# Kernel optimization log

Hardware: AMD Instinct MI355X
Metric: run time of the kernel (lower is better)

The kernel has to match this reference:

```python
import jax, jax.numpy as jnp
import numpy as np
import math

D_MODEL = 1024
D_INNER = 2048
D_HALF = D_INNER // 2
D_STATE = 16
D_CONV = 4
DT_RANK = 64
B_SZ = 4
L = 2048


def _dw_conv(x, w, b):
    # x: (b, l, c), w: (k, 1, c) depthwise, SAME padding
    y = jax.lax.conv_general_dilated(
        x, w, window_strides=(1,), padding='SAME',
        feature_group_count=x.shape[-1],
        dimension_numbers=('NWC', 'WIO', 'NWC'))
    return y + b


def _selective_scan(u, delta, A, Bc, Cc, D):
    # u, delta: (b, l, d); Bc, Cc: (b, l, n); A: (d, n); D: (d,)
    b, l, d = u.shape
    n = A.shape[1]

    def step(h, inp):
        d_t, u_t, B_t, C_t = inp  # (b,d), (b,d), (b,n), (b,n)
        dA = jnp.exp(d_t[..., None] * A)                     # (b,d,n)
        h = dA * h + (d_t * u_t)[..., None] * B_t[:, None, :]
        y = jnp.einsum('bdn,bn->bd', h, C_t)
        return h, y

    h0 = jnp.zeros((b, d, n), u.dtype)
    xs = (jnp.moveaxis(delta, 1, 0), jnp.moveaxis(u, 1, 0),
          jnp.moveaxis(Bc, 1, 0), jnp.moveaxis(Cc, 1, 0))
    _, ys = jax.lax.scan(step, h0, xs)                       # (l,b,d)
    return jnp.moveaxis(ys, 0, 1) + u * D


def setup_inputs() -> dict:
    key = jax.random.key(0)
    ks = jax.random.split(key, 12)
    x = jax.random.normal(ks[0], (B_SZ, L, D_MODEL), jnp.float32)
    W_in = jax.random.normal(ks[1], (D_MODEL, D_INNER), jnp.float32) * (D_MODEL ** -0.5)
    conv_x_w = jax.random.normal(ks[2], (D_CONV, 1, D_HALF), jnp.float32) * (D_CONV ** -0.5)
    conv_x_b = jnp.zeros((D_HALF,), jnp.float32)
    conv_z_w = jax.random.normal(ks[3], (D_CONV, 1, D_HALF), jnp.float32) * (D_CONV ** -0.5)
    conv_z_b = jnp.zeros((D_HALF,), jnp.float32)
    W_xdbl = jax.random.normal(ks[4], (D_HALF, DT_RANK + 2 * D_STATE), jnp.float32) * (D_HALF ** -0.5)
    dt_init_std = DT_RANK ** -0.5  # dt_scale = 1.0
    W_dt = jax.random.uniform(ks[5], (DT_RANK, D_HALF), jnp.float32, -dt_init_std, dt_init_std)
    rand_vals = jax.random.uniform(ks[6], (D_HALF,))
    dt_bias = jnp.exp(rand_vals * (math.log(0.1) - math.log(0.001)) + math.log(0.001))
    dt_bias = jnp.clip(dt_bias, 1e-4)
    inv_dt = dt_bias + jnp.log(-jnp.expm1(-dt_bias))
    D = jnp.ones((D_HALF,), jnp.float32)
    W_out = jax.random.normal(ks[7], (D_INNER, D_MODEL), jnp.float32) * (D_INNER ** -0.5)
    b_out = jnp.zeros((D_MODEL,), jnp.float32)
    return dict(x=x, W_in=W_in, conv_x_w=conv_x_w, conv_x_b=conv_x_b,
                conv_z_w=conv_z_w, conv_z_b=conv_z_b, W_xdbl=W_xdbl,
                W_dt=W_dt, inv_dt=inv_dt, D=D, W_out=W_out, b_out=b_out)


def reference(x, W_in, conv_x_w, conv_x_b, conv_z_w, conv_z_b, W_xdbl,
              W_dt, inv_dt, D, W_out, b_out):
    xz = x @ W_in                                            # (b,l,d_inner), no bias
    xs, z = jnp.split(xz, 2, axis=-1)                        # (b,l,d_half) each
    # A = -exp(log(arange(1..N))) tiled over channels
    A = -jnp.tile(jnp.arange(1, D_STATE + 1, dtype=jnp.float32), (D_HALF, 1))  # (d,n)
    xs = jax.nn.silu(_dw_conv(xs, conv_x_w, conv_x_b))
    z = jax.nn.silu(_dw_conv(z, conv_z_w, conv_z_b))
    x_dbl = xs @ W_xdbl                                      # (b,l,dt_rank+2n)
    dt_low, Bc, Cc = jnp.split(x_dbl, [DT_RANK, DT_RANK + D_STATE], axis=-1)
    dt = dt_low @ W_dt + inv_dt                              # Dense with bias_init=inv_dt
    delta = jax.nn.softplus(dt + inv_dt)                     # scan adds delta_bias=inv_dt again (faithful)
    y = _selective_scan(xs, delta, A, Bc, Cc, D)             # (b,l,d_half)
    y = jnp.concatenate([y, z], axis=-1)                     # (b,l,d_inner)
    return y @ W_out + b_out
```

## Files before the change

### kernel.cpp

```cpp
#include <hip/hip_runtime.h>
#include <hip/hip_bf16.h>
#include <math.h>

#define B_SZ 4
#define LSEQ 2048
#define DM 1024
#define DI 2048
#define DH 1024
#define DS 16
#define DTR 64
#define RTOT 96
#define MROWS (B_SZ * LSEQ)

#define NCH 32
#define CHUNK 64

typedef short bf8_t __attribute__((ext_vector_type(8)));
typedef float f4_t __attribute__((ext_vector_type(4)));

__device__ __forceinline__ unsigned short f2bfbits(float v) {
  __hip_bfloat16 h = __float2bfloat16(v);
  return *(unsigned short*)&h;
}

__device__ __forceinline__ void gl_lds16(const void* g, void* l) {
  __builtin_amdgcn_global_load_lds(
      (const __attribute__((address_space(1))) unsigned int*)g,
      (__attribute__((address_space(3))) unsigned int*)l,
      16, 0, 0);
}

__device__ __forceinline__ void ld8f(const float* p, unsigned short* d) {
  const float4 a = ((const float4*)p)[0];
  const float4 b = ((const float4*)p)[1];
  d[0] = f2bfbits(a.x); d[1] = f2bfbits(a.y); d[2] = f2bfbits(a.z); d[3] = f2bfbits(a.w);
  d[4] = f2bfbits(b.x); d[5] = f2bfbits(b.y); d[6] = f2bfbits(b.z); d[7] = f2bfbits(b.w);
}

__global__ void probe_kernel(const unsigned short* __restrict__ p, int* __restrict__ flag) {
  int lane = threadIdx.x;
  int sane = 0;
#pragma unroll
  for (int j = 0; j < 4; j++) {
    unsigned short lo = p[(lane * 4 + j) * 2];
    int e = (lo >> 7) & 0xFF;
    sane += (e <= 130) ? 1 : 0;
  }
  sane += __shfl_xor(sane, 1, 64);
  sane += __shfl_xor(sane, 2, 64);
  sane += __shfl_xor(sane, 4, 64);
  sane += __shfl_xor(sane, 8, 64);
  sane += __shfl_xor(sane, 16, 64);
  sane += __shfl_xor(sane, 32, 64);
  if (lane == 0) *flag = (sane >= 220) ? 1 : 0;
}

#define PREP_TOT 78848
__global__ __launch_bounds__(256) void prep_kernel(
    const int* __restrict__ flag,
    const void* s0, const void* s1, const void* s2, const void* s3,
    const void* s4, const void* s5, const void* s6, const void* s7,
    float* __restrict__ out) {
  int i = blockIdx.x * 256 + threadIdx.x;
  if (i >= PREP_TOT) return;
  const void* src; int off;
  if      (i < 4096)   { src = s0; off = i; }
  else if (i < 5120)   { src = s1; off = i - 4096; }
  else if (i < 9216)   { src = s2; off = i - 5120; }
  else if (i < 10240)  { src = s3; off = i - 9216; }
  else if (i < 75776)  { src = s4; off = i - 10240; }
  else if (i < 76800)  { src = s5; off = i - 75776; }
  else if (i < 77824)  { src = s6; off = i - 76800; }
  else                 { src = s7; off = i - 77824; }
  float v = (*flag == 1) ? __bfloat162float(((const __hip_bfloat16*)src)[off])
                         : ((const float*)src)[off];
  out[i] = v;
}

__global__ __launch_bounds__(256) void transpose_kernel(
    const int* __restrict__ flag, const void* __restrict__ W,
    unsigned short* __restrict__ Wt, int K, int N) {
  __shared__ unsigned short tile[32][33];
  int n0 = blockIdx.x * 32, k0 = blockIdx.y * 32;
  int c = threadIdx.x & 31, r8 = threadIdx.x >> 5;
  bool isbf = (*flag == 1);
#pragma unroll
  for (int p = 0; p < 4; p++) {
    int r = r8 + p * 8;
    unsigned short v;
    if (isbf) v = ((const unsigned short*)W)[(size_t)(k0 + r) * N + n0 + c];
    else      v = f2bfbits(((const float*)W)[(size_t)(k0 + r) * N + n0 + c]);
    tile[r][c] = v;
  }
  __syncthreads();
#pragma unroll
  for (int p = 0; p < 4; p++) {
    int r = r8 + p * 8;
    Wt[(size_t)(n0 + r) * K + k0 + c] = tile[c][r];
  }
}

__global__ __launch_bounds__(256) void transpose_pad_kernel(
    const int* __restrict__ flag, const void* __restrict__ W,
    unsigned short* __restrict__ Wt) {
  __shared__ unsigned short tile[32][33];
  int n0 = blockIdx.x * 32, k0 = blockIdx.y * 32;
  int c = threadIdx.x & 31, r8 = threadIdx.x >> 5;
  bool isbf = (*flag == 1);
#pragma unroll
  for (int p = 0; p < 4; p++) {
    int r = r8 + p * 8;
    unsigned short v = 0;
    if (n0 + c < RTOT) {
      if (isbf) v = ((const unsigned short*)W)[(size_t)(k0 + r) * RTOT + n0 + c];
      else      v = f2bfbits(((const float*)W)[(size_t)(k0 + r) * RTOT + n0 + c]);
    }
    tile[r][c] = v;
  }
  __syncthreads();
#pragma unroll
  for (int p = 0; p < 4; p++) {
    int r = r8 + p * 8;
    Wt[(size_t)(n0 + r) * DH + k0 + c] = tile[c][r];
  }
}

template <bool A_BF, bool O_BF>
__global__ __launch_bounds__(256) void gemm_tpl(
    const int* __restrict__ flag, int want,
    const void* __restrict__ A, const unsigned short* __restrict__ Bt,
    const float* __restrict__ bias, void* __restrict__ C,
    int M, int N, int K) {
  if (*flag != want) return;
  __shared__ __align__(16) unsigned short As[128 * 32];
  __shared__ __align__(16) unsigned short Bs[128 * 32];
  const int tid = threadIdx.x;
  const int lane = tid & 63;
  const int wave = tid >> 6;
  const int quad = lane >> 4;
  const int l16 = lane & 15;
  const int wm = (wave & 1) * 64;
  const int wn = (wave >> 1) * 64;

  const int NB = gridDim.x, MB = gridDim.y;
  int L = blockIdx.y * NB + blockIdx.x;
  int xcd = L & 7;
  int w = L >> 3;
  int m_band = xcd * (MB >> 3) + (w / NB);
  int n_blk = w % NB;
  const int m0 = m_band * 128;
  const int n0 = n_blk * 128;

  f4_t acc[4][4] = {};

  for (int k0 = 0; k0 < K; k0 += 32) {
#pragma unroll
    for (int j = 0; j < 2; j++) {
      int ch = tid + j * 256;
      int mi = ch >> 2;
      int ki = (ch & 3) ^ ((mi >> 1) & 3);
      if (A_BF) {
        gl_lds16((const unsigned short*)A + (size_t)(m0 + mi) * K + k0 + ki * 8,
                 &As[(j * 256 + wave * 64) * 8]);
      } else {
        unsigned short tmp[8];
        ld8f((const float*)A + (size_t)(m0 + mi) * K + k0 + ki * 8, tmp);
        *(uint4*)&As[ch * 8] = *(uint4*)tmp;
      }
    }
#pragma unroll
    for (int j = 0; j < 2; j++) {
      int ch = tid + j * 256;
      int ni = ch >> 2;
      int ki = (ch & 3) ^ ((ni >> 1) & 3);
      gl_lds16(Bt + (size_t)(n0 + ni) * K + k0 + ki * 8,
               &Bs[(j * 256 + wave * 64) * 8]);
    }
    __syncthreads();

    bf8_t af[4], bfr[4];
#pragma unroll
    for (int ti = 0; ti < 4; ti++) {
      int r = wm + ti * 16 + l16;
      af[ti] = *(const bf8_t*)&As[(r * 4 + (quad ^ ((r >> 1) & 3))) * 8];
    }
#pragma unroll
    for (int tj = 0; tj < 4; tj++) {
      int r = wn + tj * 16 + l16;
      bfr[tj] = *(const bf8_t*)&Bs[(r * 4 + (quad ^ ((r >> 1) & 3))) * 8];
    }
#pragma unroll
    for (int ti = 0; ti < 4; ti++)
#pragma unroll
      for (int tj = 0; tj < 4; tj++)
        acc[ti][tj] = __builtin_amdgcn_mfma_f32_16x16x32_bf16(
            af[ti], bfr[tj], acc[ti][tj], 0, 0, 0);
    __syncthreads();
  }

#pragma unroll
  for (int ti = 0; ti < 4; ti++) {
#pragma unroll
    for (int tj = 0; tj < 4; tj++) {
      int col = n0 + wn + tj * 16 + l16;
      float bv = bias ? bias[col] : 0.f;
#pragma unroll
      for (int r = 0; r < 4; r++) {
        int row = m0 + wm + ti * 16 + quad * 4 + r;
        float v = acc[ti][tj][r] + bv;
        if (O_BF) ((__hip_bfloat16*)C)[(size_t)row * N + col] = __float2bfloat16(v);
        else      ((float*)C)[(size_t)row * N + col] = v;
      }
    }
  }
}

__global__ __launch_bounds__(256) void xdbl_mfma_kernel(
    const unsigned short* __restrict__ A, const unsigned short* __restrict__ Bt,
    float* __restrict__ xdbl) {
  __shared__ __align__(16) unsigned short As[64 * 32];
  __shared__ __align__(16) unsigned short Bs[128 * 32];
  const int tid = threadIdx.x;
  const int lane = tid & 63;
  const int wave = tid >> 6;
  const int quad = lane >> 4;
  const int l16 = lane & 15;
  const int m0 = blockIdx.x * 64;

  f4_t acc[6] = {};

  for (int k0 = 0; k0 < DH; k0 += 32) {
    {
      int ch = tid;
      int mi = ch >> 2;
      int ki = (ch & 3) ^ ((mi >> 1) & 3);
      gl_lds16(A + (size_t)(m0 + mi) * DH + k0 + ki * 8, &As[(wave * 64) * 8]);
    }
#pragma unroll
    for (int j = 0; j < 2; j++) {
      int ch = tid + j * 256;
      int ni = ch >> 2;
      int ki = (ch & 3) ^ ((ni >> 1) & 3);
      gl_lds16(Bt + (size_t)ni * DH + k0 + ki * 8, &Bs[(j * 256 + wave * 64) * 8]);
    }
    __syncthreads();

    bf8_t af, bfr[6];
    {
      int r = wave * 16 + l16;
      af = *(const bf8_t*)&As[(r * 4 + (quad ^ ((r >> 1) & 3))) * 8];
    }
#pragma unroll
    for (int tj = 0; tj < 6; tj++) {
      int r = tj * 16 + l16;
      bfr[tj] = *(const bf8_t*)&Bs[(r * 4 + (quad ^ ((r >> 1) & 3))) * 8];
    }
#pragma unroll
    for (int tj = 0; tj < 6; tj++)
      acc[tj] = __builtin_amdgcn_mfma_f32_16x16x32_bf16(af, bfr[tj], acc[tj], 0, 0, 0);
    __syncthreads();
  }

#pragma unroll
  for (int tj = 0; tj < 6; tj++) {
    int col = tj * 16 + l16;
#pragma unroll
    for (int r = 0; r < 4; r++) {
      int row = m0 + wave * 16 + quad * 4 + r;
      xdbl[(size_t)row * RTOT + col] = acc[tj][r];
    }
  }
}

__global__ __launch_bounds__(256) void conv_silu_kernel(
    const __hip_bfloat16* __restrict__ xz,
    const float* __restrict__ wx, const float* __restrict__ bx,
    const float* __restrict__ wz, const float* __restrict__ bz,
    __hip_bfloat16* __restrict__ xs_bf, __hip_bfloat16* __restrict__ cat) {
  int gid = blockIdx.x * 256 + threadIdx.x;
  int c = gid & 1023;
  int m = gid >> 10;
  int t = m & (LSEQ - 1);
  float ax = bx[c];
  float az = bz[c];
#pragma unroll
  for (int j = 0; j < 4; j++) {
    int tt = t - 1 + j;
    if (tt < 0 || tt >= LSEQ) continue;
    size_t row = (size_t)(m - t + tt);
    float vx = __bfloat162float(xz[row * DI + c]);
    float vz = __bfloat162float(xz[row * DI + DH + c]);
    ax += wx[j * DH + c] * vx;
    az += wz[j * DH + c] * vz;
  }
  float sx = ax / (1.f + __expf(-ax));
  float sz = az / (1.f + __expf(-az));
  xs_bf[(size_t)m * DH + c] = __float2bfloat16(sx);
  cat[(size_t)m * DI + DH + c] = __float2bfloat16(sz);
}

__global__ __launch_bounds__(256) void delta_kernel(
    const float* __restrict__ xdbl, const float* __restrict__ Wdt,
    const float* __restrict__ inv_dt, float* __restrict__ delta) {
  const int d = blockIdx.x * 256 + threadIdx.x;
  const int m0 = blockIdx.y * 8;
  __shared__ float xr[8][DTR];
#pragma unroll
  for (int i = 0; i < 2; i++) {
    int e = threadIdx.x + i * 256;
    xr[e >> 6][e & 63] = xdbl[(size_t)(m0 + (e >> 6)) * RTOT + (e & 63)];
  }
  __syncthreads();
  float acc[8];
#pragma unroll
  for (int i = 0; i < 8; i++) acc[i] = 0.f;
  for (int rr = 0; rr < DTR; rr++) {
    float w = Wdt[(size_t)rr * DH + d];
#pragma unroll
    for (int i = 0; i < 8; i++) acc[i] = fmaf(xr[i][rr], w, acc[i]);
  }
  const float bias2 = 2.f * inv_dt[d];
#pragma unroll
  for (int i = 0; i < 8; i++) {
    float v = acc[i] + bias2;
    float sp = (v > 0.f) ? (v + log1pf(__expf(-v))) : log1pf(__expf(v));
    delta[(size_t)(m0 + i) * DH + d] = sp;
  }
}

__global__ __launch_bounds__(256) void scan_pass1(
    const float* __restrict__ delta, const __hip_bfloat16* __restrict__ u,
    const float* __restrict__ xdbl,
    float* __restrict__ Echunks, float* __restrict__ hp) {
  const int tid = threadIdx.x;
  const int d = blockIdx.x * 256 + tid;
  const int c = blockIdx.y, b = blockIdx.z;
  const int row0 = b * LSEQ + c * CHUNK;
  __shared__ float sBC[CHUNK][32];
#pragma unroll
  for (int i = 0; i < 2; i++) {
    int task = tid + i * 256;
    int r = task >> 3, seg = task & 7;
    *(float4*)&sBC[r][seg * 4] =
        *(const float4*)&xdbl[(size_t)(row0 + r) * RTOT + DTR + seg * 4];
  }
  __syncthreads();
  float h[16];
#pragma unroll
  for (int n = 0; n < 16; n++) h[n] = 0.f;
  float E = 1.f;
  for (int t = 0; t < CHUNK; t++) {
    size_t off = (size_t)(row0 + t) * DH + d;
    float dt = delta[off];
    float ut = __bfloat162float(u[off]);
    float e = __expf(-dt);
    E *= e;
    float du = dt * ut;
    float p = 1.f;
#pragma unroll
    for (int n = 0; n < 16; n++) {
      p *= e;
      h[n] = fmaf(p, h[n], du * sBC[t][n]);
    }
  }
  Echunks[((size_t)c * B_SZ + b) * DH + d] = E;
#pragma unroll
  for (int n = 0; n < 16; n++)
    hp[(((size_t)c * B_SZ + b) * 16 + n) * DH + d] = h[n];
}

__global__ __launch_bounds__(256) void scan_pass2(
    const float* __restrict__ Echunks, const float* __restrict__ hp,
    float* __restrict__ hs) {
  int t = blockIdx.x * 256 + threadIdx.x;
  int d = t & 1023;
  int n = (t >> 10) & 15;
  int b = t >> 14;
  float h = 0.f;
  const int k0 = n + 1;
  for (int c = 0; c < NCH; c++) {
    float E = Echunks[((size_t)c * B_SZ + b) * DH + d];
    float a = 1.f, base = E;
    int k = k0;
#pragma unroll
    for (int i = 0; i < 5; i++) {
      if (k & 1) a *= base;
      base *= base;
      k >>= 1;
    }
    size_t idx = (((size_t)c * B_SZ + b) * 16 + n) * DH + d;
    hs[idx] = h;
    h = fmaf(a, h, hp[idx]);
  }
}

__global__ __launch_bounds__(256) void scan_pass3(
    const float* __restrict__ delta, const __hip_bfloat16* __restrict__ u,
    const float* __restrict__ xdbl, const float* __restrict__ hs,
    const float* __restrict__ Dvec, __hip_bfloat16* __restrict__ cat) {
  const int tid = threadIdx.x;
  const int d = blockIdx.x * 256 + tid;
  const int c = blockIdx.y, b = blockIdx.z;
  const int row0 = b * LSEQ + c * CHUNK;
  __shared__ float sBC[CHUNK][32];
#pragma unroll
  for (int i = 0; i < 2; i++) {
    int task = tid + i * 256;
    int r = task >> 3, seg = task & 7;
    *(float4*)&sBC[r][seg * 4] =
        *(const float4*)&xdbl[(size_t)(row0 + r) * RTOT + DTR + seg * 4];
  }
  __syncthreads();
  float h[16];
#pragma unroll
  for (int n = 0; n < 16; n++)
    h[n] = hs[(((size_t)c * B_SZ + b) * 16 + n) * DH + d];
  const float Dd = Dvec[d];
  for (int t = 0; t < CHUNK; t++) {
    size_t off = (size_t)(row0 + t) * DH + d;
    float dt = delta[off];
    float ut = __bfloat162float(u[off]);
    float e = __expf(-dt);
    float du = dt * ut;
    float p = 1.f, y = 0.f;
#pragma unroll
    for (int n = 0; n < 16; n++) {
      p *= e;
      h[n] = fmaf(p, h[n], du * sBC[t][n]);
      y = fmaf(h[n], sBC[t][16 + n], y);
    }
    y = fmaf(ut, Dd, y);
    cat[(size_t)(row0 + t) * DI + d] = __float2bfloat16(y);
  }
}

extern "C" void kernel_launch(void* const* d_in, const int* in_sizes, int n_in,
                              void* d_out, int out_size, void* d_ws, size_t ws_size,
                              hipStream_t stream) {
  char* ws = (char*)d_ws;
  __hip_bfloat16* xz  = (__hip_bfloat16*)(ws);
  float* delta        = (float*)(ws);
  __hip_bfloat16* xs  = (__hip_bfloat16*)(ws + ((size_t)32 << 20));
  __hip_bfloat16* cat = (__hip_bfloat16*)(ws + ((size_t)64 << 20));
  float* xdbl         = (float*)(ws + ((size_t)96 << 20));
  float* Echunks      = (float*)(ws + ((size_t)99 << 20));
  float* hp           = (float*)(ws + ((size_t)100 << 20));
  float* hs           = (float*)(ws + ((size_t)108 << 20));
  unsigned short* Wt_in  = (unsigned short*)(ws + ((size_t)116 << 20));
  unsigned short* Wt_out = (unsigned short*)(ws + ((size_t)120 << 20));
  unsigned short* Wxt    = (unsigned short*)(ws + ((size_t)124 << 20));
  float* cw           = (float*)(ws + ((size_t)125 << 20));
  int* flag           = (int*)(ws + ((size_t)126 << 20));

  const float* conv_xwf = cw + 0;
  const float* conv_xbf = cw + 4096;
  const float* conv_zwf = cw + 5120;
  const float* conv_zbf = cw + 9216;
  const float* Wdtf     = cw + 10240;
  const float* inv_dtf  = cw + 75776;
  const float* Df       = cw + 76800;
  const float* b_outf   = cw + 77824;

  probe_kernel<<<1, 64, 0, stream>>>((const unsigned short*)d_in[0], flag);
  prep_kernel<<<(PREP_TOT + 255) / 256, 256, 0, stream>>>(
      flag, d_in[2], d_in[3], d_in[4], d_in[5], d_in[7], d_in[8], d_in[9],
      d_in[11], cw);
  transpose_kernel<<<dim3(DI / 32, DM / 32), 256, 0, stream>>>(
      flag, d_in[1], Wt_in, DM, DI);
  transpose_kernel<<<dim3(DM / 32, DI / 32), 256, 0, stream>>>(
      flag, d_in[10], Wt_out, DI, DM);
  transpose_pad_kernel<<<dim3(4, DH / 32), 256, 0, stream>>>(flag, d_in[6], Wxt);

  gemm_tpl<true, true><<<dim3(DI / 128, MROWS / 128), 256, 0, stream>>>(
      flag, 1, d_in[0], Wt_in, (const float*)nullptr, xz, MROWS, DI, DM);
  gemm_tpl<false, true><<<dim3(DI / 128, MROWS / 128), 256, 0, stream>>>(
      flag, 0, d_in[0], Wt_in, (const float*)nullptr, xz, MROWS, DI, DM);
  conv_silu_kernel<<<(MROWS * DH) / 256, 256, 0, stream>>>(
      xz, conv_xwf, conv_xbf, conv_zwf, conv_zbf, xs, cat);
  xdbl_mfma_kernel<<<MROWS / 64, 256, 0, stream>>>(
      (const unsigned short*)xs, Wxt, xdbl);
  delta_kernel<<<dim3(4, MROWS / 8), 256, 0, stream>>>(xdbl, Wdtf, inv_dtf, delta);
  scan_pass1<<<dim3(4, NCH, B_SZ), 256, 0, stream>>>(delta, xs, xdbl, Echunks, hp);
  scan_pass2<<<256, 256, 0, stream>>>(Echunks, hp, hs);
  scan_pass3<<<dim3(4, NCH, B_SZ), 256, 0, stream>>>(delta, xs, xdbl, hs, Df, cat);
  gemm_tpl<true, true><<<dim3(DM / 128, MROWS / 128), 256, 0, stream>>>(
      flag, 1, cat, Wt_out, b_outf, d_out, MROWS, DM, DI);
  gemm_tpl<true, false><<<dim3(DM / 128, MROWS / 128), 256, 0, stream>>>(
      flag, 0, cat, Wt_out, b_outf, d_out, MROWS, DM, DI);
}
```

Before: 414.2 us.

## Deepen GEMM K-tile, vectorize conv, pack bf16 delta with u for scan

Measured after the change: 380.2 us. -8.2%, faster.

```diff
diff --git a/kernel.cpp b/kernel.cpp
--- a/kernel.cpp
+++ b/kernel.cpp
@@ -21,6 +21,14 @@
 __device__ __forceinline__ unsigned short f2bfbits(float v) {
   __hip_bfloat16 h = __float2bfloat16(v);
   return *(unsigned short*)&h;
+}
+__device__ __forceinline__ float bfu_lo(unsigned int v) {
+  unsigned int x = v << 16;
+  return *(float*)&x;
+}
+__device__ __forceinline__ float bfu_hi(unsigned int v) {
+  unsigned int x = v & 0xffff0000u;
+  return *(float*)&x;
 }
 
 __device__ __forceinline__ void gl_lds16(const void* g, void* l) {
@@ -132,8 +140,8 @@
     const float* __restrict__ bias, void* __restrict__ C,
     int M, int N, int K) {
   if (*flag != want) return;
-  __shared__ __align__(16) unsigned short As[128 * 32];
-  __shared__ __align__(16) unsigned short Bs[128 * 32];
+  __shared__ __align__(16) unsigned short As[128 * 64];
+  __shared__ __align__(16) unsigned short Bs[128 * 64];
   const int tid = threadIdx.x;
   const int lane = tid & 63;
   const int wave = tid >> 6;
@@ -153,12 +161,13 @@
 
   f4_t acc[4][4] = {};
 
-  for (int k0 = 0; k0 < K; k0 += 32) {
-#pragma unroll
-    for (int j = 0; j < 2; j++) {
+  for (int k0 = 0; k0 < K; k0 += 64) {
+#pragma unroll
+    for (int j = 0; j < 4; j++) {
       int ch = tid + j * 256;
-      int mi = ch >> 2;
-      int ki = (ch & 3) ^ ((mi >> 1) & 3);
+      int mi = ch >> 3;
+      int s = ch & 7;
+      int ki = (s & 4) | ((s & 3) ^ ((mi >> 1) & 3));
       if (A_BF) {
         gl_lds16((const unsigned short*)A + (size_t)(m0 + mi) * K + k0 + ki * 8,
                  &As[(j * 256 + wave * 64) * 8]);
@@ -169,32 +178,36 @@
       }
     }
 #pragma unroll
-    for (int j = 0; j < 2; j++) {
+    for (int j = 0; j < 4; j++) {
       int ch = tid + j * 256;
-      int ni = ch >> 2;
-      int ki = (ch & 3) ^ ((ni >> 1) & 3);
+      int ni = ch >> 3;
+      int s = ch & 7;
+      int ki = (s & 4) | ((s & 3) ^ ((ni >> 1) & 3));
       gl_lds16(Bt + (size_t)(n0 + ni) * K + k0 + ki * 8,
                &Bs[(j * 256 + wave * 64) * 8]);
     }
     __syncthreads();
 
-    bf8_t af[4], bfr[4];
-#pragma unroll
-    for (int ti = 0; ti < 4; ti++) {
-      int r = wm + ti * 16 + l16;
-      af[ti] = *(const bf8_t*)&As[(r * 4 + (quad ^ ((r >> 1) & 3))) * 8];
-    }
-#pragma unroll
-    for (int tj = 0; tj < 4; tj++) {
-      int r = wn + tj * 16 + l16;
-      bfr[tj] = *(const bf8_t*)&Bs[(r * 4 + (quad ^ ((r >> 1) & 3))) * 8];
-    }
-#pragma unroll
-    for (int ti = 0; ti < 4; ti++)
-#pragma unroll
-      for (int tj = 0; tj < 4; tj++)
-        acc[ti][tj] = __builtin_amdgcn_mfma_f32_16x16x32_bf16(
-            af[ti], bfr[tj], acc[ti][tj], 0, 0, 0);
+#pragma unroll
+    for (int h = 0; h < 2; h++) {
+      bf8_t af[4], bfr[4];
+#pragma unroll
+      for (int ti = 0; ti < 4; ti++) {
+        int r = wm + ti * 16 + l16;
+        af[ti] = *(const bf8_t*)&As[(r * 8 + h * 4 + (quad ^ ((r >> 1) & 3))) * 8];
+      }
+#pragma unroll
+      for (int tj = 0; tj < 4; tj++) {
+        int r = wn + tj * 16 + l16;
+        bfr[tj] = *(const bf8_t*)&Bs[(r * 8 + h * 4 + (quad ^ ((r >> 1) & 3))) * 8];
+      }
+#pragma unroll
+      for (int ti = 0; ti < 4; ti++)
+#pragma unroll
+        for (int tj = 0; tj < 4; tj++)
+          acc[ti][tj] = __builtin_amdgcn_mfma_f32_16x16x32_bf16(
+              af[ti], bfr[tj], acc[ti][tj], 0, 0, 0);
+    }
     __syncthreads();
   }
 
@@ -273,35 +286,53 @@
 }
 
 __global__ __launch_bounds__(256) void conv_silu_kernel(
-    const __hip_bfloat16* __restrict__ xz,
+    const unsigned short* __restrict__ xz,
     const float* __restrict__ wx, const float* __restrict__ bx,
     const float* __restrict__ wz, const float* __restrict__ bz,
-    __hip_bfloat16* __restrict__ xs_bf, __hip_bfloat16* __restrict__ cat) {
+    unsigned short* __restrict__ xs_bf, unsigned short* __restrict__ cat) {
   int gid = blockIdx.x * 256 + threadIdx.x;
-  int c = gid & 1023;
-  int m = gid >> 10;
+  int cg = gid & 127;
+  int c0 = cg * 8;
+  int m = gid >> 7;
   int t = m & (LSEQ - 1);
-  float ax = bx[c];
-  float az = bz[c];
+  float ax[8], az[8];
+#pragma unroll
+  for (int i = 0; i < 8; i++) { ax[i] = bx[c0 + i]; az[i] = bz[c0 + i]; }
 #pragma unroll
   for (int j = 0; j < 4; j++) {
     int tt = t - 1 + j;
     if (tt < 0 || tt >= LSEQ) continue;
     size_t row = (size_t)(m - t + tt);
-    float vx = __bfloat162float(xz[row * DI + c]);
-    float vz = __bfloat162float(xz[row * DI + DH + c]);
-    ax += wx[j * DH + c] * vx;
-    az += wz[j * DH + c] * vz;
-  }
-  float sx = ax / (1.f + __expf(-ax));
-  float sz = az / (1.f + __expf(-az));
-  xs_bf[(size_t)m * DH + c] = __float2bfloat16(sx);
-  cat[(size_t)m * DI + DH + c] = __float2bfloat16(sz);
+    uint4 vx = *(const uint4*)&xz[row * DI + c0];
+    uint4 vz = *(const uint4*)&xz[row * DI + DH + c0];
+    const unsigned int* px = (const unsigned int*)&vx;
+    const unsigned int* pz = (const unsigned int*)&vz;
+#pragma unroll
+    for (int q = 0; q < 4; q++) {
+      float x0 = bfu_lo(px[q]), x1 = bfu_hi(px[q]);
+      float z0 = bfu_lo(pz[q]), z1 = bfu_hi(pz[q]);
+      ax[q * 2]     = fmaf(wx[j * DH + c0 + q * 2], x0, ax[q * 2]);
+      ax[q * 2 + 1] = fmaf(wx[j * DH + c0 + q * 2 + 1], x1, ax[q * 2 + 1]);
+      az[q * 2]     = fmaf(wz[j * DH + c0 + q * 2], z0, az[q * 2]);
+      az[q * 2 + 1] = fmaf(wz[j * DH + c0 + q * 2 + 1], z1, az[q * 2 + 1]);
+    }
+  }
+  unsigned short sx[8], sz[8];
+#pragma unroll
+  for (int i = 0; i < 8; i++) {
+    float vx = ax[i] / (1.f + __expf(-ax[i]));
+    float vz = az[i] / (1.f + __expf(-az[i]));
+    sx[i] = f2bfbits(vx);
+    sz[i] = f2bfbits(vz);
+  }
+  *(uint4*)&xs_bf[(size_t)m * DH + c0] = *(uint4*)sx;
+  *(uint4*)&cat[(size_t)m * DI + DH + c0] = *(uint4*)sz;
 }
 
 __global__ __launch_bounds__(256) void delta_kernel(
     const float* __restrict__ xdbl, const float* __restrict__ Wdt,
-    const float* __restrict__ inv_dt, float* __restrict__ delta) {
+    const float* __restrict__ inv_dt, const unsigned short* __restrict__ xs,
+    unsigned int* __restrict__ du) {
   const int d = blockIdx.x * 256 + threadIdx.x;
   const int m0 = blockIdx.y * 8;
   __shared__ float xr[8][DTR];
@@ -324,13 +355,14 @@
   for (int i = 0; i < 8; i++) {
     float v = acc[i] + bias2;
     float sp = (v > 0.f) ? (v + log1pf(__expf(-v))) : log1pf(__expf(v));
-    delta[(size_t)(m0 + i) * DH + d] = sp;
+    unsigned int lo = f2bfbits(sp);
+    unsigned int hi = xs[(size_t)(m0 + i) * DH + d];
+    du[(size_t)(m0 + i) * DH + d] = lo | (hi << 16);
   }
 }
 
 __global__ __launch_bounds__(256) void scan_pass1(
-    const float* __restrict__ delta, const __hip_bfloat16* __restrict__ u,
-    const float* __restrict__ xdbl,
+    const unsigned int* __restrict__ du, const float* __restrict__ xdbl,
     float* __restrict__ Echunks, float* __restrict__ hp) {
   const int tid = threadIdx.x;
   const int d = blockIdx.x * 256 + tid;
@@ -350,17 +382,16 @@
   for (int n = 0; n < 16; n++) h[n] = 0.f;
   float E = 1.f;
   for (int t = 0; t < CHUNK; t++) {
-    size_t off = (size_t)(row0 + t) * DH + d;
-    float dt = delta[off];
-    float ut = __bfloat162float(u[off]);
+    unsigned int v = du[(size_t)(row0 + t) * DH + d];
+    float dt = bfu_lo(v), ut = bfu_hi(v);
     float e = __expf(-dt);
     E *= e;
-    float du = dt * ut;
+    float dv = dt * ut;
     float p = 1.f;
 #pragma unroll
     for (int n = 0; n < 16; n++) {
       p *= e;
-      h[n] = fmaf(p, h[n], du * sBC[t][n]);
+      h[n] = fmaf(p, h[n], dv * sBC[t][n]);
     }
   }
   Echunks[((size_t)c * B_SZ + b) * DH + d] = E;
@@ -395,9 +426,9 @@
 }
 
 __global__ __launch_bounds__(256) void scan_pass3(
-    const float* __restrict__ delta, const __hip_bfloat16* __restrict__ u,
-    const float* __restrict__ xdbl, const float* __restrict__ hs,
-    const float* __restrict__ Dvec, __hip_bfloat16* __restrict__ cat) {
+    const unsigned int* __restrict__ du, const float* __restrict__ xdbl,
+    const float* __restrict__ hs, const float* __restrict__ Dvec,
+    __hip_bfloat16* __restrict__ cat) {
   const int tid = threadIdx.x;
   const int d = blockIdx.x * 256 + tid;
   const int c = blockIdx.y, b = blockIdx.z;
@@ -417,16 +448,15 @@
     h[n] = hs[(((size_t)c * B_SZ + b) * 16 + n) * DH + d];
   const float Dd = Dvec[d];
   for (int t = 0; t < CHUNK; t++) {
-    size_t off = (size_t)(row0 + t) * DH + d;
-    float dt = delta[off];
-    float ut = __bfloat162float(u[off]);
+    unsigned int v = du[(size_t)(row0 + t) * DH + d];
+    float dt = bfu_lo(v), ut = bfu_hi(v);
     float e = __expf(-dt);
-    float du = dt * ut;
+    float dv = dt * ut;
     float p = 1.f, y = 0.f;
 #pragma unroll
     for (int n = 0; n < 16; n++) {
       p *= e;
-      h[n] = fmaf(p, h[n], du * sBC[t][n]);
+      h[n] = fmaf(p, h[n], dv * sBC[t][n]);
       y = fmaf(h[n], sBC[t][16 + n], y);
     }
     y = fmaf(ut, Dd, y);
@@ -439,7 +469,7 @@
                               hipStream_t stream) {
   char* ws = (char*)d_ws;
   __hip_bfloat16* xz  = (__hip_bfloat16*)(ws);
-  float* delta        = (float*)(ws);
+  unsigned int* du    = (unsigned int*)(ws);
   __hip_bfloat16* xs  = (__hip_bfloat16*)(ws + ((size_t)32 << 20));
   __hip_bfloat16* cat = (__hip_bfloat16*)(ws + ((size_t)64 << 20));
   float* xdbl         = (float*)(ws + ((size_t)96 << 20));
@@ -475,14 +505,16 @@
       flag, 1, d_in[0], Wt_in, (const float*)nullptr, xz, MROWS, DI, DM);
   gemm_tpl<false, true><<<dim3(DI / 128, MROWS / 128), 256, 0, stream>>>(
       flag, 0, d_in[0], Wt_in, (const float*)nullptr, xz, MROWS, DI, DM);
-  conv_silu_kernel<<<(MROWS * DH) / 256, 256, 0, stream>>>(
-      xz, conv_xwf, conv_xbf, conv_zwf, conv_zbf, xs, cat);
+  conv_silu_kernel<<<(MROWS * 128) / 256, 256, 0, stream>>>(
+      (const unsigned short*)xz, conv_xwf, conv_xbf, conv_zwf, conv_zbf,
+      (unsigned short*)xs, (unsigned short*)cat);
   xdbl_mfma_kernel<<<MROWS / 64, 256, 0, stream>>>(
       (const unsigned short*)xs, Wxt, xdbl);
-  delta_kernel<<<dim3(4, MROWS / 8), 256, 0, stream>>>(xdbl, Wdtf, inv_dtf, delta);
-  scan_pass1<<<dim3(4, NCH, B_SZ), 256, 0, stream>>>(delta, xs, xdbl, Echunks, hp);
+  delta_kernel<<<dim3(4, MROWS / 8), 256, 0, stream>>>(
+      xdbl, Wdtf, inv_dtf, (const unsigned short*)xs, du);
+  scan_pass1<<<dim3(4, NCH, B_SZ), 256, 0, stream>>>(du, xdbl, Echunks, hp);
   scan_pass2<<<256, 256, 0, stream>>>(Echunks, hp, hs);
-  scan_pass3<<<dim3(4, NCH, B_SZ), 256, 0, stream>>>(delta, xs, xdbl, hs, Df, cat);
+  scan_pass3<<<dim3(4, NCH, B_SZ), 256, 0, stream>>>(du, xdbl, hs, Df, cat);
   gemm_tpl<true, true><<<dim3(DM / 128, MROWS / 128), 256, 0, stream>>>(
       flag, 1, cat, Wt_out, b_outf, d_out, MROWS, DM, DI);
   gemm_tpl<true, false><<<dim3(DM / 128, MROWS / 128), 256, 0, stream>>>(
```
